# Kernel tuning notes

Hardware: AMD Instinct MI355X
Metric: run time of the kernel (lower is better)

## Reference

```python
import jax, jax.numpy as jnp
import numpy as np

NUM_HEADS = 16
ROPE_THETA = 10000.0


def _rope_angles(seq_len, head_dim, dtype):
    # lucidrains rotary_embedding_torch: freqs = theta^(-2i/d) for i in 0..d/2,
    # angles = pos * freq, then each angle repeated twice along last dim (interleaved pairs).
    inv_freq = 1.0 / (ROPE_THETA ** (jnp.arange(0, head_dim, 2, dtype=jnp.float32) / head_dim))
    angles = jnp.arange(seq_len, dtype=jnp.float32)[:, None] * inv_freq  # [N, D/2]
    return jnp.repeat(angles, 2, axis=-1).astype(dtype)  # [N, D]


def _rotate_half(t):
    # interleaved pairs: (x0, x1) -> (-x1, x0)
    t1 = t[..., ::2]
    t2 = t[..., 1::2]
    return jnp.stack([-t2, t1], axis=-1).reshape(t.shape)


def _apply_rope(t, cos, sin):
    # t: [B, H, N, D]; cos/sin: [N, D]
    return t * cos + _rotate_half(t) * sin


def setup_inputs() -> dict:
    key = jax.random.key(0)
    ks = jax.random.split(key, 5)
    B, N, C = 4, 1024, 1024
    return {
        "x": jax.random.normal(ks[0], (B, N, C), dtype=jnp.float32),
        "w_qkv": jax.random.normal(ks[1], (C, 3 * C), dtype=jnp.float32) * (C ** -0.5),
        "b_qkv": jax.random.normal(ks[2], (3 * C,), dtype=jnp.float32) * 0.02,
        "w_proj": jax.random.normal(ks[3], (C, C), dtype=jnp.float32) * (C ** -0.5),
        "b_proj": jax.random.normal(ks[4], (C,), dtype=jnp.float32) * 0.02,
    }


def reference(x, w_qkv, b_qkv, w_proj, b_proj):
    B, N, C = x.shape
    H = NUM_HEADS
    D = C // H

    qkv = x @ w_qkv + b_qkv  # [B, N, 3C]
    qkv = qkv.reshape(B, N, 3, H, D).transpose(2, 0, 3, 1, 4)  # [3, B, H, N, D]
    q, k, v = qkv[0], qkv[1], qkv[2]

    ang = _rope_angles(N, D, x.dtype)
    cos, sin = jnp.cos(ang), jnp.sin(ang)
    q = _apply_rope(q, cos, sin)
    k = _apply_rope(k, cos, sin)

    scale = D ** -0.5  # SDPA default scale
    scores = jnp.einsum("bhqd,bhkd->bhqk", q, k) * scale
    attn = jax.nn.softmax(scores, axis=-1)
    out = jnp.einsum("bhqk,bhkd->bhqd", attn, v)  # [B, H, N, D]

    out = out.transpose(0, 2, 1, 3).reshape(B, N, C)
    return out @ w_proj + b_proj
```

## Files before the change

### kernel.cpp

```cpp
#include <hip/hip_runtime.h>
#include <math.h>

#define BB 4
#define NN 1024
#define CC 1024
#define HH 16
#define DD 64
#define N3 3072

typedef __attribute__((ext_vector_type(8))) short bf16x8;
typedef __attribute__((ext_vector_type(8))) _Float16 f16x8;
typedef __attribute__((ext_vector_type(4))) _Float16 f16x4;
typedef __attribute__((ext_vector_type(4))) float f32x4;
typedef __attribute__((ext_vector_type(4))) unsigned int u32x4;

struct ushort4_t { unsigned short x, y, z, w; };

static __device__ __forceinline__ unsigned short f2b(float f) {
    union { float f; unsigned int u; } v; v.f = f;
    unsigned int r = (v.u + 0x7fffu + ((v.u >> 16) & 1u)) >> 16;
    return (unsigned short)r;
}

static __device__ __forceinline__ void ldg_lds16(const void* g, void* l) {
    __builtin_amdgcn_global_load_lds(
        (const __attribute__((address_space(1))) unsigned int*)g,
        (__attribute__((address_space(3))) unsigned int*)l, 16, 0, 0);
}

__global__ __launch_bounds__(256) void prep(const float* __restrict__ x,
                                            const float* __restrict__ wq,
                                            const float* __restrict__ wp,
                                            _Float16* __restrict__ Xh,
                                            _Float16* __restrict__ Wqt,
                                            _Float16* __restrict__ Wpt,
                                            float* __restrict__ ct,
                                            float* __restrict__ st) {
    const int blk = blockIdx.x;
    const int t = threadIdx.x;
    if (blk < 4096) {
        int tid = blk * 256 + t;
        float4 v = ((const float4*)x)[tid];
        f16x4 o = {(_Float16)v.x, (_Float16)v.y, (_Float16)v.z, (_Float16)v.w};
        ((f16x4*)Xh)[tid] = o;
    } else if (blk < 5632) {
        int idx = blk - 4096;
        int n  = (idx % 12) * 256 + t;
        int k0 = (idx / 12) * 8;
        f16x8 o;
        #pragma unroll
        for (int kk = 0; kk < 8; kk++)
            o[kk] = (_Float16)wq[(size_t)(k0 + kk) * N3 + n];
        *(f16x8*)(Wqt + (size_t)n * 1024 + k0) = o;
    } else if (blk < 6144) {
        int idx = blk - 5632;
        int n  = (idx % 4) * 256 + t;
        int k0 = (idx / 4) * 8;
        f16x8 o;
        #pragma unroll
        for (int kk = 0; kk < 8; kk++)
            o[kk] = (_Float16)wp[(size_t)(k0 + kk) * 1024 + n];
        *(f16x8*)(Wpt + (size_t)n * 1024 + k0) = o;
    } else {
        int tid = (blk - 6144) * 256 + t;
        int n = tid >> 5, i = tid & 31;
        double ang = (double)n * exp2(-(double)i * (13.287712379549449 / 32.0));
        ct[tid] = (float)cos(ang);
        st[tid] = (float)sin(ang);
    }
}

static __device__ __forceinline__ void gemm_body_pipe(const char* gA, const char* gB,
                                                      int m0, int n0,
                                                      _Float16* As0, _Float16* As1,
                                                      _Float16* Bs0, _Float16* Bs1,
                                                      int tid, int ln, int qd,
                                                      int wm, int wn, f32x4 acc[4][4]) {
    const int lrow   = tid >> 3;
    const int lchunk = tid & 7;
    const int swz    = (lchunk ^ (lrow & 7)) * 8;

    u32x4 pa[4], pb[4];

    #pragma unroll
    for (int c = 0; c < 4; c++) {
        size_t ra = (size_t)(m0 + c * 32 + lrow) * 2048 + lchunk * 16;
        size_t rb = (size_t)(n0 + c * 32 + lrow) * 2048 + lchunk * 16;
        pa[c] = *(const u32x4*)(gA + ra);
        pb[c] = *(const u32x4*)(gB + rb);
    }
    #pragma unroll
    for (int c = 0; c < 4; c++) {
        *(u32x4*)&As0[(c * 32 + lrow) * 64 + swz] = pa[c];
        *(u32x4*)&Bs0[(c * 32 + lrow) * 64 + swz] = pb[c];
    }
    #pragma unroll
    for (int c = 0; c < 4; c++) {
        size_t ra = (size_t)(m0 + c * 32 + lrow) * 2048 + 128 + lchunk * 16;
        size_t rb = (size_t)(n0 + c * 32 + lrow) * 2048 + 128 + lchunk * 16;
        pa[c] = *(const u32x4*)(gA + ra);
        pb[c] = *(const u32x4*)(gB + rb);
    }
    __syncthreads();

    #pragma unroll
    for (int t = 0; t < 16; t++) {
        const _Float16* Ac = (t & 1) ? As1 : As0;
        const _Float16* Bc = (t & 1) ? Bs1 : Bs0;

        #pragma unroll
        for (int kc = 0; kc < 2; kc++) {
            f16x8 af[4], bf[4];
            #pragma unroll
            for (int i = 0; i < 4; i++)
                af[i] = *(const f16x8*)&Ac[(wm + i * 16 + ln) * 64 +
                                           (((kc * 4 + qd) ^ (ln & 7)) * 8)];
            #pragma unroll
            for (int j = 0; j < 4; j++)
                bf[j] = *(const f16x8*)&Bc[(wn + j * 16 + ln) * 64 +
                                           (((kc * 4 + qd) ^ (ln & 7)) * 8)];
            #pragma unroll
            for (int i = 0; i < 4; i++)
                #pragma unroll
                for (int j = 0; j < 4; j++)
                    acc[i][j] = __builtin_amdgcn_mfma_f32_16x16x32_f16(af[i], bf[j],
                                                                       acc[i][j], 0, 0, 0);
        }

        if (t < 15) {
            _Float16* An = (t & 1) ? As0 : As1;
            _Float16* Bn = (t & 1) ? Bs0 : Bs1;
            #pragma unroll
            for (int c = 0; c < 4; c++) {
                *(u32x4*)&An[(c * 32 + lrow) * 64 + swz] = pa[c];
                *(u32x4*)&Bn[(c * 32 + lrow) * 64 + swz] = pb[c];
            }
            if (t < 14) {
                size_t ko = (size_t)(t + 2) * 128;
                #pragma unroll
                for (int c = 0; c < 4; c++) {
                    size_t ra = (size_t)(m0 + c * 32 + lrow) * 2048 + ko + lchunk * 16;
                    size_t rb = (size_t)(n0 + c * 32 + lrow) * 2048 + ko + lchunk * 16;
                    pa[c] = *(const u32x4*)(gA + ra);
                    pb[c] = *(const u32x4*)(gB + rb);
                }
            }
        }
        __syncthreads();
    }
}

__global__ __launch_bounds__(256) void qkv_mfma(const _Float16* __restrict__ Ah,
                                                const _Float16* __restrict__ Bt,
                                                const float* __restrict__ bias,
                                                const float* __restrict__ cost,
                                                const float* __restrict__ sint,
                                                unsigned short* __restrict__ Q,
                                                unsigned short* __restrict__ K,
                                                unsigned short* __restrict__ Vtg) {
    __shared__ __align__(16) _Float16 As[2][128 * 64];
    __shared__ __align__(16) _Float16 Bs[2][128 * 64];
    const int t = threadIdx.x;
    const int lane = t & 63;
    const int w = t >> 6;
    const int ln = lane & 15, qd = lane >> 4;
    const int n0 = blockIdx.x * 128;
    const int m0 = blockIdx.y * 128;
    const int wm = (w >> 1) * 64, wn = (w & 1) * 64;

    f32x4 acc[4][4];
    #pragma unroll
    for (int i = 0; i < 4; i++)
        #pragma unroll
        for (int j = 0; j < 4; j++) acc[i][j] = (f32x4){0.f, 0.f, 0.f, 0.f};

    gemm_body_pipe((const char*)Ah, (const char*)Bt, m0, n0,
                   As[0], As[1], Bs[0], Bs[1], t, ln, qd, wm, wn, acc);

    const int s = n0 >> 10;
    const int h = ((n0 + wn) >> 6) & 15;
    if (s < 2) {
        unsigned short* dst = (s == 0) ? Q : K;
        const float sc0 = (s == 0) ? 0.125f : 1.0f;
        #pragma unroll
        for (int i = 0; i < 4; i++) {
            #pragma unroll
            for (int reg = 0; reg < 4; reg++) {
                int row = m0 + wm + i * 16 + qd * 4 + reg;
                int b = row >> 10, n = row & 1023;
                size_t obase = (((size_t)(b * HH + h)) * NN + n) * DD;
                #pragma unroll
                for (int j = 0; j < 4; j++) {
                    int d = j * 16 + ln;
                    float v = acc[i][j][reg] + bias[n0 + wn + d];
                    float pv = __shfl_xor(v, 1);
                    float cs = cost[n * 32 + (d >> 1)];
                    float sn = sint[n * 32 + (d >> 1)];
                    float outv = ((d & 1) ? (v * cs + pv * sn) : (v * cs - pv * sn)) * sc0;
                    dst[obase + d] = f2b(outv);
                }
            }
        }
    } else {
        #pragma unroll
        for (int i = 0; i < 4; i++) {
            int row0 = m0 + wm + i * 16 + qd * 4;
            int b = row0 >> 10, n = row0 & 1023;
            size_t tbase = ((size_t)(b * HH + h)) * DD * NN + n;
            #pragma unroll
            for (int j = 0; j < 4; j++) {
                int d = j * 16 + ln;
                float bb = bias[n0 + wn + d];
                ushort4_t pk;
                pk.x = f2b(acc[i][j][0] + bb);
                pk.y = f2b(acc[i][j][1] + bb);
                pk.z = f2b(acc[i][j][2] + bb);
                pk.w = f2b(acc[i][j][3] + bb);
                *(ushort4_t*)&Vtg[tbase + (size_t)d * NN] = pk;
            }
        }
    }
}

__global__ __launch_bounds__(256) void attn_flash(const unsigned short* __restrict__ Qb,
                                                  const unsigned short* __restrict__ Kb,
                                                  const unsigned short* __restrict__ Vtg,
                                                  _Float16* __restrict__ AO) {
    __shared__ __align__(16) unsigned short Ks[3][64 * 64];
    __shared__ __align__(16) unsigned short Vt[2][64 * 64];
    __shared__ __align__(16) unsigned short Ps[4][16 * 64];

    const int t    = threadIdx.x;
    const int lane = t & 63;
    const int w    = t >> 6;
    const int ln   = lane & 15;
    const int qd   = lane >> 4;
    const int bq   = blockIdx.x;
    const int h    = blockIdx.y;
    const int b    = blockIdx.z;
    const size_t base = (size_t)(b * HH + h) * NN * DD;
    const char* Kc = (const char*)(Kb + base);
    const char* Vc = (const char*)(Vtg + base);
    const int xorc = ((lane & 7) ^ (lane >> 3)) * 16;
    const int r8   = lane >> 3;
    const int wrow = w * 16;

    bf16x8 qf0, qf1;
    {
        const unsigned short* qp = Qb + base + (size_t)(bq * 64 + wrow + ln) * DD + qd * 8;
        qf0 = *(const bf16x8*)qp;
        qf1 = *(const bf16x8*)(qp + 32);
    }

    f32x4 o[5];
    #pragma unroll
    for (int x = 0; x < 5; x++) o[x] = (f32x4){0.f, 0.f, 0.f, 0.f};

    bf16x8 onesf;
    #pragma unroll
    for (int x = 0; x < 8; x++) onesf[x] = (short)0x3F80;

    #pragma unroll
    for (int tile = 0; tile < 3; tile++)
        #pragma unroll
        for (int c = 0; c < 2; c++) {
            int rr = wrow + c * 8 + r8;
            ldg_lds16(Kc + (size_t)(tile * 64 + rr) * 128 + xorc,
                      &Ks[tile][(wrow + c * 8) * 64]);
        }
    #pragma unroll
    for (int tile = 0; tile < 2; tile++)
        #pragma unroll
        for (int c = 0; c < 2; c++) {
            int rr = wrow + c * 8 + r8;
            ldg_lds16(Vc + (size_t)rr * 2048 + (size_t)tile * 128 + xorc,
                      &Vt[tile][(wrow + c * 8) * 64]);
        }
    __syncthreads();

    f32x4 scur[4];
    {
        const unsigned short* KsB = Ks[0];
        #pragma unroll
        for (int j = 0; j < 4; j++) {
            f32x4 sj = {0.f, 0.f, 0.f, 0.f};
            bf16x8 k0f = *(const bf16x8*)&KsB[(ln + 16 * j) * 64 + ((qd ^ (ln & 7)) * 8)];
            bf16x8 k1f = *(const bf16x8*)&KsB[(ln + 16 * j) * 64 + (((4 + qd) ^ (ln & 7)) * 8)];
            sj = __builtin_amdgcn_mfma_f32_16x16x32_bf16(qf0, k0f, sj, 0, 0, 0);
            sj = __builtin_amdgcn_mfma_f32_16x16x32_bf16(qf1, k1f, sj, 0, 0, 0);
            scur[j] = sj;
        }
    }

    const float C1 = 1.44269504f;
    const float C0 = -16.0f * 1.44269504f;

    #pragma unroll
    for (int tt = 0; tt < 16; tt++) {
        f32x4 snext[4];
        if (tt < 15) {
            const unsigned short* KsB = Ks[(tt + 1) % 3];
            #pragma unroll
            for (int j = 0; j < 4; j++) {
                f32x4 sj = {0.f, 0.f, 0.f, 0.f};
                bf16x8 k0f = *(const bf16x8*)&KsB[(ln + 16 * j) * 64 + ((qd ^ (ln & 7)) * 8)];
                bf16x8 k1f = *(const bf16x8*)&KsB[(ln + 16 * j) * 64 + (((4 + qd) ^ (ln & 7)) * 8)];
                sj = __builtin_amdgcn_mfma_f32_16x16x32_bf16(qf0, k0f, sj, 0, 0, 0);
                sj = __builtin_amdgcn_mfma_f32_16x16x32_bf16(qf1, k1f, sj, 0, 0, 0);
                snext[j] = sj;
            }
        }

        unsigned short* PsB = &Ps[w][0];
        #pragma unroll
        for (int j = 0; j < 4; j++) {
            #pragma unroll
            for (int r = 0; r < 4; r++) {
                float p = exp2f(fmaf(scur[j][r], C1, C0));
                union { float f; unsigned int u; } cv; cv.f = p;
                int m = qd * 4 + r;
                PsB[m * 64 + ((((ln >> 3) + 2 * j) ^ (m & 7)) * 8) + (ln & 7)] =
                    (unsigned short)((cv.u + 0x8000u) >> 16);
            }
        }

        {
            const unsigned short* VtB = Vt[tt & 1];
            bf16x8 pf0 = *(const bf16x8*)&PsB[ln * 64 + ((qd ^ (ln & 7)) * 8)];
            bf16x8 pf1 = *(const bf16x8*)&PsB[ln * 64 + (((4 + qd) ^ (ln & 7)) * 8)];
            #pragma unroll
            for (int j = 0; j < 4; j++) {
                bf16x8 v0f = *(const bf16x8*)&VtB[(ln + 16 * j) * 64 + ((qd ^ (ln & 7)) * 8)];
                bf16x8 v1f = *(const bf16x8*)&VtB[(ln + 16 * j) * 64 + (((4 + qd) ^ (ln & 7)) * 8)];
                o[j] = __builtin_amdgcn_mfma_f32_16x16x32_bf16(pf0, v0f, o[j], 0, 0, 0);
                o[j] = __builtin_amdgcn_mfma_f32_16x16x32_bf16(pf1, v1f, o[j], 0, 0, 0);
            }
            o[4] = __builtin_amdgcn_mfma_f32_16x16x32_bf16(pf0, onesf, o[4], 0, 0, 0);
            o[4] = __builtin_amdgcn_mfma_f32_16x16x32_bf16(pf1, onesf, o[4], 0, 0, 0);
        }

        __syncthreads();

        if (tt <= 12) {
            int tile = tt + 3;
            #pragma unroll
            for (int c = 0; c < 2; c++) {
                int rr = wrow + c * 8 + r8;
                ldg_lds16(Kc + (size_t)(tile * 64 + rr) * 128 + xorc,
                          &Ks[tt % 3][(wrow + c * 8) * 64]);
            }
        }
        if (tt <= 13) {
            int tile = tt + 2;
            #pragma unroll
            for (int c = 0; c < 2; c++) {
                int rr = wrow + c * 8 + r8;
                ldg_lds16(Vc + (size_t)rr * 2048 + (size_t)tile * 128 + xorc,
                          &Vt[tt & 1][(wrow + c * 8) * 64]);
            }
        }

        #pragma unroll
        for (int j = 0; j < 4; j++) scur[j] = snext[j];
    }

    #pragma unroll
    for (int r = 0; r < 4; r++) {
        float inv = 1.0f / o[4][r];
        int q = bq * 64 + wrow + qd * 4 + r;
        _Float16* op = AO + (((size_t)b * NN + q) * HH + h) * DD + ln;
        op[0]  = (_Float16)(o[0][r] * inv);
        op[16] = (_Float16)(o[1][r] * inv);
        op[32] = (_Float16)(o[2][r] * inv);
        op[48] = (_Float16)(o[3][r] * inv);
    }
}

__global__ __launch_bounds__(256) void proj_mfma(const _Float16* __restrict__ Ah,
                                                 const _Float16* __restrict__ Bt,
                                                 const float* __restrict__ bias,
                                                 float* __restrict__ out) {
    __shared__ __align__(16) _Float16 As[2][128 * 64];
    __shared__ __align__(16) _Float16 Bs[2][128 * 64];
    const int t = threadIdx.x;
    const int lane = t & 63;
    const int w = t >> 6;
    const int ln = lane & 15, qd = lane >> 4;
    const int n0 = blockIdx.x * 128;
    const int m0 = blockIdx.y * 128;
    const int wm = (w >> 1) * 64, wn = (w & 1) * 64;

    f32x4 acc[4][4];
    #pragma unroll
    for (int i = 0; i < 4; i++)
        #pragma unroll
        for (int j = 0; j < 4; j++) acc[i][j] = (f32x4){0.f, 0.f, 0.f, 0.f};

    gemm_body_pipe((const char*)Ah, (const char*)Bt, m0, n0,
                   As[0], As[1], Bs[0], Bs[1], t, ln, qd, wm, wn, acc);

    #pragma unroll
    for (int i = 0; i < 4; i++) {
        #pragma unroll
        for (int reg = 0; reg < 4; reg++) {
            int row = m0 + wm + i * 16 + qd * 4 + reg;
            #pragma unroll
            for (int j = 0; j < 4; j++) {
                int col = n0 + wn + j * 16 + ln;
                out[(size_t)row * 1024 + col] = acc[i][j][reg] + bias[col];
            }
        }
    }
}

extern "C" void kernel_launch(void* const* d_in, const int* in_sizes, int n_in,
                              void* d_out, int out_size, void* d_ws, size_t ws_size,
                              hipStream_t stream) {
    const float* x      = (const float*)d_in[0];
    const float* w_qkv  = (const float*)d_in[1];
    const float* b_qkv  = (const float*)d_in[2];
    const float* w_proj = (const float*)d_in[3];
    const float* b_proj = (const float*)d_in[4];
    float* out = (float*)d_out;

    char* ws = (char*)d_ws;
    _Float16* Xh   = (_Float16*)(ws);
    _Float16* Wqt  = (_Float16*)(ws + (8u << 20));
    _Float16* Wpt  = (_Float16*)(ws + (14u << 20));
    unsigned short* Q  = (unsigned short*)(ws + (16u << 20));
    unsigned short* K  = (unsigned short*)(ws + (24u << 20));
    unsigned short* Vt = (unsigned short*)(ws + (32u << 20));
    _Float16* AOh  = (_Float16*)(ws + (40u << 20));
    float* cost    = (float*)(ws + (48u << 20));
    float* sint    = (float*)(ws + (48u << 20) + (128u << 10));

    prep<<<6272, 256, 0, stream>>>(x, w_qkv, w_proj, Xh, Wqt, Wpt, cost, sint);
    qkv_mfma<<<dim3(24, 32), 256, 0, stream>>>(Xh, Wqt, b_qkv, cost, sint, Q, K, Vt);
    attn_flash<<<dim3(16, 16, 4), 256, 0, stream>>>(Q, K, Vt, AOh);
    proj_mfma<<<dim3(8, 32), 256, 0, stream>>>(AOh, Wpt, b_proj, out);
}
```

Baseline: 185.7 us.

## Double query rows per attention block and narrow projection GEMM tiles

The attention kernel now gives each wave two 16-row query groups, so a block covers 128 queries. Each K/V tile loaded into LDS is reused across twice as many queries, and the grid is halved. The projection GEMM switches to 128x64 output tiles with a new pipelined body, doubling its grid from 256 to 512 blocks to fill the CUs better. The cost is more registers per attention thread (double the accumulators and scores), which may lower occupancy, and fewer attention blocks.

Result: no change. 182.3 us (-1.8%).

```diff
diff --git a/kernel.cpp b/kernel.cpp
--- a/kernel.cpp
+++ b/kernel.cpp
@@ -150,6 +150,85 @@
     }
 }
 
+static __device__ __forceinline__ void gemm_body_pipe_n64(const char* gA, const char* gB,
+                                                          int m0, int n0,
+                                                          _Float16* As0, _Float16* As1,
+                                                          _Float16* Bs0, _Float16* Bs1,
+                                                          int tid, int ln, int qd,
+                                                          int wm, int wn, f32x4 acc[4][2]) {
+    const int lrow   = tid >> 3;
+    const int lchunk = tid & 7;
+    const int swz    = (lchunk ^ (lrow & 7)) * 8;
+
+    u32x4 pa[4], pb[2];
+
+    #pragma unroll
+    for (int c = 0; c < 4; c++)
+        pa[c] = *(const u32x4*)(gA + (size_t)(m0 + c * 32 + lrow) * 2048 + lchunk * 16);
+    #pragma unroll
+    for (int c = 0; c < 2; c++)
+        pb[c] = *(const u32x4*)(gB + (size_t)(n0 + c * 32 + lrow) * 2048 + lchunk * 16);
+    #pragma unroll
+    for (int c = 0; c < 4; c++)
+        *(u32x4*)&As0[(c * 32 + lrow) * 64 + swz] = pa[c];
+    #pragma unroll
+    for (int c = 0; c < 2; c++)
+        *(u32x4*)&Bs0[(c * 32 + lrow) * 64 + swz] = pb[c];
+    #pragma unroll
+    for (int c = 0; c < 4; c++)
+        pa[c] = *(const u32x4*)(gA + (size_t)(m0 + c * 32 + lrow) * 2048 + 128 + lchunk * 16);
+    #pragma unroll
+    for (int c = 0; c < 2; c++)
+        pb[c] = *(const u32x4*)(gB + (size_t)(n0 + c * 32 + lrow) * 2048 + 128 + lchunk * 16);
+    __syncthreads();
+
+    #pragma unroll
+    for (int t = 0; t < 16; t++) {
+        const _Float16* Ac = (t & 1) ? As1 : As0;
+        const _Float16* Bc = (t & 1) ? Bs1 : Bs0;
+
+        #pragma unroll
+        for (int kc = 0; kc < 2; kc++) {
+            f16x8 af[4], bf[2];
+            #pragma unroll
+            for (int i = 0; i < 4; i++)
+                af[i] = *(const f16x8*)&Ac[(wm + i * 16 + ln) * 64 +
+                                           (((kc * 4 + qd) ^ (ln & 7)) * 8)];
+            #pragma unroll
+            for (int j = 0; j < 2; j++)
+                bf[j] = *(const f16x8*)&Bc[(wn + j * 16 + ln) * 64 +
+                                           (((kc * 4 + qd) ^ (ln & 7)) * 8)];
+            #pragma unroll
+            for (int i = 0; i < 4; i++)
+                #pragma unroll
+                for (int j = 0; j < 2; j++)
+                    acc[i][j] = __builtin_amdgcn_mfma_f32_16x16x32_f16(af[i], bf[j],
+                                                                       acc[i][j], 0, 0, 0);
+        }
+
+        if (t < 15) {
+            _Float16* An = (t & 1) ? As0 : As1;
+            _Float16* Bn = (t & 1) ? Bs0 : Bs1;
+            #pragma unroll
+            for (int c = 0; c < 4; c++)
+                *(u32x4*)&An[(c * 32 + lrow) * 64 + swz] = pa[c];
+            #pragma unroll
+            for (int c = 0; c < 2; c++)
+                *(u32x4*)&Bn[(c * 32 + lrow) * 64 + swz] = pb[c];
+            if (t < 14) {
+                size_t ko = (size_t)(t + 2) * 128;
+                #pragma unroll
+                for (int c = 0; c < 4; c++)
+                    pa[c] = *(const u32x4*)(gA + (size_t)(m0 + c * 32 + lrow) * 2048 + ko + lchunk * 16);
+                #pragma unroll
+                for (int c = 0; c < 2; c++)
+                    pb[c] = *(const u32x4*)(gB + (size_t)(n0 + c * 32 + lrow) * 2048 + ko + lchunk * 16);
+            }
+        }
+        __syncthreads();
+    }
+}
+
 __global__ __launch_bounds__(256) void qkv_mfma(const _Float16* __restrict__ Ah,
                                                 const _Float16* __restrict__ Bt,
                                                 const float* __restrict__ bias,
@@ -228,7 +307,7 @@
                                                   _Float16* __restrict__ AO) {
     __shared__ __align__(16) unsigned short Ks[3][64 * 64];
     __shared__ __align__(16) unsigned short Vt[2][64 * 64];
-    __shared__ __align__(16) unsigned short Ps[4][16 * 64];
+    __shared__ __align__(16) unsigned short Ps[4][32 * 64];
 
     const int t    = threadIdx.x;
     const int lane = t & 63;
@@ -245,16 +324,20 @@
     const int r8   = lane >> 3;
     const int wrow = w * 16;
 
-    bf16x8 qf0, qf1;
-    {
-        const unsigned short* qp = Qb + base + (size_t)(bq * 64 + wrow + ln) * DD + qd * 8;
-        qf0 = *(const bf16x8*)qp;
-        qf1 = *(const bf16x8*)(qp + 32);
-    }
-
-    f32x4 o[5];
-    #pragma unroll
-    for (int x = 0; x < 5; x++) o[x] = (f32x4){0.f, 0.f, 0.f, 0.f};
+    bf16x8 qf[2][2];
+    #pragma unroll
+    for (int g = 0; g < 2; g++) {
+        const unsigned short* qp = Qb + base +
+            (size_t)(bq * 128 + w * 32 + g * 16 + ln) * DD + qd * 8;
+        qf[g][0] = *(const bf16x8*)qp;
+        qf[g][1] = *(const bf16x8*)(qp + 32);
+    }
+
+    f32x4 o[2][5];
+    #pragma unroll
+    for (int g = 0; g < 2; g++)
+        #pragma unroll
+        for (int x = 0; x < 5; x++) o[g][x] = (f32x4){0.f, 0.f, 0.f, 0.f};
 
     bf16x8 onesf;
     #pragma unroll
@@ -278,17 +361,20 @@
         }
     __syncthreads();
 
-    f32x4 scur[4];
+    f32x4 scur[2][4];
     {
         const unsigned short* KsB = Ks[0];
         #pragma unroll
         for (int j = 0; j < 4; j++) {
-            f32x4 sj = {0.f, 0.f, 0.f, 0.f};
             bf16x8 k0f = *(const bf16x8*)&KsB[(ln + 16 * j) * 64 + ((qd ^ (ln & 7)) * 8)];
             bf16x8 k1f = *(const bf16x8*)&KsB[(ln + 16 * j) * 64 + (((4 + qd) ^ (ln & 7)) * 8)];
-            sj = __builtin_amdgcn_mfma_f32_16x16x32_bf16(qf0, k0f, sj, 0, 0, 0);
-            sj = __builtin_amdgcn_mfma_f32_16x16x32_bf16(qf1, k1f, sj, 0, 0, 0);
-            scur[j] = sj;
+            #pragma unroll
+            for (int g = 0; g < 2; g++) {
+                f32x4 sj = {0.f, 0.f, 0.f, 0.f};
+                sj = __builtin_amdgcn_mfma_f32_16x16x32_bf16(qf[g][0], k0f, sj, 0, 0, 0);
+                sj = __builtin_amdgcn_mfma_f32_16x16x32_bf16(qf[g][1], k1f, sj, 0, 0, 0);
+                scur[g][j] = sj;
+            }
         }
     }
 
@@ -297,46 +383,60 @@
 
     #pragma unroll
     for (int tt = 0; tt < 16; tt++) {
-        f32x4 snext[4];
+        f32x4 snext[2][4];
         if (tt < 15) {
             const unsigned short* KsB = Ks[(tt + 1) % 3];
             #pragma unroll
             for (int j = 0; j < 4; j++) {
-                f32x4 sj = {0.f, 0.f, 0.f, 0.f};
                 bf16x8 k0f = *(const bf16x8*)&KsB[(ln + 16 * j) * 64 + ((qd ^ (ln & 7)) * 8)];
                 bf16x8 k1f = *(const bf16x8*)&KsB[(ln + 16 * j) * 64 + (((4 + qd) ^ (ln & 7)) * 8)];
-                sj = __builtin_amdgcn_mfma_f32_16x16x32_bf16(qf0, k0f, sj, 0, 0, 0);
-                sj = __builtin_amdgcn_mfma_f32_16x16x32_bf16(qf1, k1f, sj, 0, 0, 0);
-                snext[j] = sj;
+                #pragma unroll
+                for (int g = 0; g < 2; g++) {
+                    f32x4 sj = {0.f, 0.f, 0.f, 0.f};
+                    sj = __builtin_amdgcn_mfma_f32_16x16x32_bf16(qf[g][0], k0f, sj, 0, 0, 0);
+                    sj = __builtin_amdgcn_mfma_f32_16x16x32_bf16(qf[g][1], k1f, sj, 0, 0, 0);
+                    snext[g][j] = sj;
+                }
             }
         }
 
         unsigned short* PsB = &Ps[w][0];
         #pragma unroll
-        for (int j = 0; j < 4; j++) {
-            #pragma unroll
-            for (int r = 0; r < 4; r++) {
-                float p = exp2f(fmaf(scur[j][r], C1, C0));
-                union { float f; unsigned int u; } cv; cv.f = p;
-                int m = qd * 4 + r;
-                PsB[m * 64 + ((((ln >> 3) + 2 * j) ^ (m & 7)) * 8) + (ln & 7)] =
-                    (unsigned short)((cv.u + 0x8000u) >> 16);
-            }
-        }
+        for (int g = 0; g < 2; g++)
+            #pragma unroll
+            for (int j = 0; j < 4; j++)
+                #pragma unroll
+                for (int r = 0; r < 4; r++) {
+                    float p = exp2f(fmaf(scur[g][j][r], C1, C0));
+                    union { float f; unsigned int u; } cv; cv.f = p;
+                    int m = g * 16 + qd * 4 + r;
+                    PsB[m * 64 + ((((ln >> 3) + 2 * j) ^ (m & 7)) * 8) + (ln & 7)] =
+                        (unsigned short)((cv.u + 0x8000u) >> 16);
+                }
 
         {
             const unsigned short* VtB = Vt[tt & 1];
-            bf16x8 pf0 = *(const bf16x8*)&PsB[ln * 64 + ((qd ^ (ln & 7)) * 8)];
-            bf16x8 pf1 = *(const bf16x8*)&PsB[ln * 64 + (((4 + qd) ^ (ln & 7)) * 8)];
+            bf16x8 pf[2][2];
+            #pragma unroll
+            for (int g = 0; g < 2; g++) {
+                pf[g][0] = *(const bf16x8*)&PsB[(g * 16 + ln) * 64 + ((qd ^ (ln & 7)) * 8)];
+                pf[g][1] = *(const bf16x8*)&PsB[(g * 16 + ln) * 64 + (((4 + qd) ^ (ln & 7)) * 8)];
+            }
             #pragma unroll
             for (int j = 0; j < 4; j++) {
                 bf16x8 v0f = *(const bf16x8*)&VtB[(ln + 16 * j) * 64 + ((qd ^ (ln & 7)) * 8)];
                 bf16x8 v1f = *(const bf16x8*)&VtB[(ln + 16 * j) * 64 + (((4 + qd) ^ (ln & 7)) * 8)];
-                o[j] = __builtin_amdgcn_mfma_f32_16x16x32_bf16(pf0, v0f, o[j], 0, 0, 0);
-                o[j] = __builtin_amdgcn_mfma_f32_16x16x32_bf16(pf1, v1f, o[j], 0, 0, 0);
-            }
-            o[4] = __builtin_amdgcn_mfma_f32_16x16x32_bf16(pf0, onesf, o[4], 0, 0, 0);
-            o[4] = __builtin_amdgcn_mfma_f32_16x16x32_bf16(pf1, onesf, o[4], 0, 0, 0);
+                #pragma unroll
+                for (int g = 0; g < 2; g++) {
+                    o[g][j] = __builtin_amdgcn_mfma_f32_16x16x32_bf16(pf[g][0], v0f, o[g][j], 0, 0, 0);
+                    o[g][j] = __builtin_amdgcn_mfma_f32_16x16x32_bf16(pf[g][1], v1f, o[g][j], 0, 0, 0);
+                }
+            }
+            #pragma unroll
+            for (int g = 0; g < 2; g++) {
+                o[g][4] = __builtin_amdgcn_mfma_f32_16x16x32_bf16(pf[g][0], onesf, o[g][4], 0, 0, 0);
+                o[g][4] = __builtin_amdgcn_mfma_f32_16x16x32_bf16(pf[g][1], onesf, o[g][4], 0, 0, 0);
+            }
         }
 
         __syncthreads();
@@ -361,19 +461,23 @@
         }
 
         #pragma unroll
-        for (int j = 0; j < 4; j++) scur[j] = snext[j];
-    }
-
-    #pragma unroll
-    for (int r = 0; r < 4; r++) {
-        float inv = 1.0f / o[4][r];
-        int q = bq * 64 + wrow + qd * 4 + r;
-        _Float16* op = AO + (((size_t)b * NN + q) * HH + h) * DD + ln;
-        op[0]  = (_Float16)(o[0][r] * inv);
-        op[16] = (_Float16)(o[1][r] * inv);
-        op[32] = (_Float16)(o[2][r] * inv);
-        op[48] = (_Float16)(o[3][r] * inv);
-    }
+        for (int g = 0; g < 2; g++)
+            #pragma unroll
+            for (int j = 0; j < 4; j++) scur[g][j] = snext[g][j];
+    }
+
+    #pragma unroll
+    for (int g = 0; g < 2; g++)
+        #pragma unroll
+        for (int r = 0; r < 4; r++) {
+            float inv = 1.0f / o[g][4][r];
+            int q = bq * 128 + w * 32 + g * 16 + qd * 4 + r;
+            _Float16* op = AO + (((size_t)b * NN + q) * HH + h) * DD + ln;
+            op[0]  = (_Float16)(o[g][0][r] * inv);
+            op[16] = (_Float16)(o[g][1][r] * inv);
+            op[32] = (_Float16)(o[g][2][r] * inv);
+            op[48] = (_Float16)(o[g][3][r] * inv);
+        }
 }
 
 __global__ __launch_bounds__(256) void proj_mfma(const _Float16* __restrict__ Ah,
@@ -381,23 +485,23 @@
                                                  const float* __restrict__ bias,
                                                  float* __restrict__ out) {
     __shared__ __align__(16) _Float16 As[2][128 * 64];
-    __shared__ __align__(16) _Float16 Bs[2][128 * 64];
+    __shared__ __align__(16) _Float16 Bs[2][64 * 64];
     const int t = threadIdx.x;
     const int lane = t & 63;
     const int w = t >> 6;
     const int ln = lane & 15, qd = lane >> 4;
-    const int n0 = blockIdx.x * 128;
+    const int n0 = blockIdx.x * 64;
     const int m0 = blockIdx.y * 128;
-    const int wm = (w >> 1) * 64, wn = (w & 1) * 64;
-
-    f32x4 acc[4][4];
+    const int wm = (w >> 1) * 64, wn = (w & 1) * 32;
+
+    f32x4 acc[4][2];
     #pragma unroll
     for (int i = 0; i < 4; i++)
         #pragma unroll
-        for (int j = 0; j < 4; j++) acc[i][j] = (f32x4){0.f, 0.f, 0.f, 0.f};
-
-    gemm_body_pipe((const char*)Ah, (const char*)Bt, m0, n0,
-                   As[0], As[1], Bs[0], Bs[1], t, ln, qd, wm, wn, acc);
+        for (int j = 0; j < 2; j++) acc[i][j] = (f32x4){0.f, 0.f, 0.f, 0.f};
+
+    gemm_body_pipe_n64((const char*)Ah, (const char*)Bt, m0, n0,
+                       As[0], As[1], Bs[0], Bs[1], t, ln, qd, wm, wn, acc);
 
     #pragma unroll
     for (int i = 0; i < 4; i++) {
@@ -405,7 +509,7 @@
         for (int reg = 0; reg < 4; reg++) {
             int row = m0 + wm + i * 16 + qd * 4 + reg;
             #pragma unroll
-            for (int j = 0; j < 4; j++) {
+            for (int j = 0; j < 2; j++) {
                 int col = n0 + wn + j * 16 + ln;
                 out[(size_t)row * 1024 + col] = acc[i][j][reg] + bias[col];
             }
@@ -436,6 +540,6 @@
 
     prep<<<6272, 256, 0, stream>>>(x, w_qkv, w_proj, Xh, Wqt, Wpt, cost, sint);
     qkv_mfma<<<dim3(24, 32), 256, 0, stream>>>(Xh, Wqt, b_qkv, cost, sint, Q, K, Vt);
-    attn_flash<<<dim3(16, 16, 4), 256, 0, stream>>>(Q, K, Vt, AOh);
-    proj_mfma<<<dim3(8, 32), 256, 0, stream>>>(AOh, Wpt, b_proj, out);
-}
+    attn_flash<<<dim3(8, 16, 4), 256, 0, stream>>>(Q, K, Vt, AOh);
+    proj_mfma<<<dim3(16, 32), 256, 0, stream>>>(AOh, Wpt, b_proj, out);
+}
```
